# Optimization experiments

Hardware: AMD Instinct MI355X
Metric: run time of the kernel (lower is better)

## Reference

```python
import jax, jax.numpy as jnp
import numpy as np

NUM_CODES = 8192
CODE_DIM = 64
DECAY = 0.99
EPSILON = 1e-05
COMMITMENT_COST = 0.25


def setup_inputs() -> dict:
    key = jax.random.key(0)
    k1, k2, k3 = jax.random.split(key, 3)
    z = jax.random.normal(k1, (32768, CODE_DIM), dtype=jnp.float32)
    emb = jax.random.normal(k2, (NUM_CODES, CODE_DIM), dtype=jnp.float32)
    emb = emb / jnp.linalg.norm(emb, axis=1, keepdims=True)
    return {
        "z": z,
        "embedding": emb,
        "ema_cluster_size": jnp.zeros((NUM_CODES,), dtype=jnp.float32),
        "ema_embedding": emb.copy(),
    }


def reference(z, embedding, ema_cluster_size, ema_embedding):
    z_flat = z.reshape(-1, CODE_DIM)  # [N, D]
    # squared euclidean distances [N, K]
    distances = (
        jnp.sum(z_flat * z_flat, axis=1, keepdims=True)
        - 2.0 * (z_flat @ embedding.T)
        + jnp.sum(embedding * embedding, axis=1)
    )
    indices = jnp.argmin(distances, axis=1)  # [N] int
    z_q = embedding[indices]  # [N, D] gather

    # EMA buffer updates (training path), expressed as pure outputs.
    counts = jax.ops.segment_sum(
        jnp.ones_like(indices, dtype=z_flat.dtype), indices, num_segments=NUM_CODES
    )  # encodings.sum(0)
    dw = jax.ops.segment_sum(z_flat, indices, num_segments=NUM_CODES)  # encodings.T @ z_flat
    new_cluster_size = DECAY * ema_cluster_size + (1.0 - DECAY) * counts
    new_ema_embedding = DECAY * ema_embedding + (1.0 - DECAY) * dw
    n = jnp.sum(new_cluster_size)
    cluster_size = (new_cluster_size + EPSILON) / (n + NUM_CODES * EPSILON) * n
    new_embedding = new_ema_embedding / cluster_size[:, None]

    z_q_full = z_q.reshape(z.shape)
    z_q_st = z + jax.lax.stop_gradient(z_q_full - z)  # straight-through
    vq_loss = COMMITMENT_COST * jnp.mean(
        (jax.lax.stop_gradient(z_q_full) - z) ** 2
    )
    return (z_q_st, indices, vq_loss, new_embedding, new_cluster_size, new_ema_embedding)
```

## Files before the change

kernel.cpp:

```cpp
#include <hip/hip_runtime.h>

typedef _Float16 half8 __attribute__((ext_vector_type(8)));
typedef float f32x4 __attribute__((ext_vector_type(4)));

#define N_PTS   32768
#define DIMS    64
#define K_CODES 8192

#define OUT_ZQ      0
#define OUT_IDX     2097152
#define OUT_LOSS    2129920
#define OUT_NEWEMB  2129921
#define OUT_NCS     2654209
#define OUT_NEWEMA  2662401

#define SC_EHI      0
#define SC_ELO      262144
#define SC_ENSC     524288
#define SC_VAL1     532480
#define SC_IDX1     794624
#define SC_VAL2     1056768
#define SC_FIXLIST  1318912
#define SC_SORTED   1323008
#define SC_OFFSETS  1355776

#define WS_COUNTS   0
#define WS_CURSOR   8192
#define WS_LOSS     16384
#define WS_NSUM     16385
#define WS_FIXCNT   16386
#define WS_ZERO_BYTES (16388u * 4u)
#define WS_NCS      16388
#define WS_ENORM    24580
#define WS_IDX      32772
#define WS_DW       65540

#define MARGIN_SCALED 16.0f

__device__ inline void gld16(const void* g, void* l) {
    __builtin_amdgcn_global_load_lds((const __attribute__((address_space(1))) unsigned*)g,
                                     (__attribute__((address_space(3))) unsigned*)l, 16, 0, 0);
}
__device__ inline void gld4(const void* g, void* l) {
    __builtin_amdgcn_global_load_lds((const __attribute__((address_space(1))) unsigned*)g,
                                     (__attribute__((address_space(3))) unsigned*)l, 4, 0, 0);
}

__global__ __launch_bounds__(256) void esplit_kernel(const float* __restrict__ emb,
                                                     float4* __restrict__ ehi4,
                                                     float4* __restrict__ elo4,
                                                     float* __restrict__ ensc,
                                                     float* __restrict__ enorm) {
    int k = blockIdx.x * 256 + threadIdx.x;
    const float4* e4 = reinterpret_cast<const float4*>(emb + (size_t)k * DIMS);
    float vals[64];
    float sum = 0.0f;
#pragma unroll
    for (int i = 0; i < 16; ++i) {
        float4 v = e4[i];
        vals[i*4+0] = v.x; vals[i*4+1] = v.y; vals[i*4+2] = v.z; vals[i*4+3] = v.w;
        sum = fmaf(v.x, v.x, sum); sum = fmaf(v.y, v.y, sum);
        sum = fmaf(v.z, v.z, sum); sum = fmaf(v.w, v.w, sum);
    }
    enorm[k] = sum;
    ensc[k]  = 65536.0f * sum;
#pragma unroll
    for (int c = 0; c < 8; ++c) {
        union { _Float16 h[8]; float4 v; } uh, ul;
#pragma unroll
        for (int j = 0; j < 8; ++j) {
            float X = 256.0f * vals[c*8+j];
            _Float16 hh = (_Float16)X;
            uh.h[j] = hh;
            ul.h[j] = (_Float16)(X - (float)hh);
        }
        int cc = c ^ (k & 7);
        ehi4[(size_t)k*8 + cc] = uh.v;
        elo4[(size_t)k*8 + cc] = ul.v;
    }
}

__global__ __launch_bounds__(256) void argmin_mfma(const float* __restrict__ z,
                                                   const char* __restrict__ ehi_g,
                                                   const char* __restrict__ elo_g,
                                                   const float* __restrict__ ensc_g,
                                                   float* __restrict__ val1,
                                                   int* __restrict__ idx1,
                                                   float* __restrict__ val2) {
    __shared__ __align__(16) char ebuf[2][2][8192];
    __shared__ float enb[2][64];

    const int tid = threadIdx.x;
    const int w   = tid >> 6;
    const int l   = tid & 63;
    const int l15 = l & 15;
    const int l4  = l >> 4;
    const int bid = blockIdx.x;
    const int rowbase = (bid >> 2) * 128 + w * 32;
    const int c0      = (bid & 3) * 2048;

    half8 ahi[2][2], alo[2][2];
#pragma unroll
    for (int s = 0; s < 2; ++s) {
        const float* zp = z + (size_t)(rowbase + s*16 + l15) * DIMS + l4 * 8;
#pragma unroll
        for (int ks = 0; ks < 2; ++ks) {
            float4 z0 = *reinterpret_cast<const float4*>(zp + ks*32);
            float4 z1 = *reinterpret_cast<const float4*>(zp + ks*32 + 4);
            float xv[8] = {z0.x, z0.y, z0.z, z0.w, z1.x, z1.y, z1.z, z1.w};
            half8 h, lo;
#pragma unroll
            for (int j = 0; j < 8; ++j) {
                float X = -512.0f * xv[j];
                _Float16 hh = (_Float16)X;
                h[j]  = hh;
                lo[j] = (_Float16)(X - (float)hh);
            }
            ahi[s][ks] = h; alo[s][ks] = lo;
        }
    }

    float b1[8], b2[8]; int i1[8];
#pragma unroll
    for (int r = 0; r < 8; ++r) { b1[r] = 3.4e38f; b2[r] = 3.4e38f; i1[r] = 0; }

    int rdoff[2];
#pragma unroll
    for (int ks = 0; ks < 2; ++ks)
        rdoff[ks] = l15 * 128 + (((ks*4 + l4) ^ (l15 & 7)) * 16);

    {
        const size_t gb = (size_t)c0 * 128;
        const char* sh = ehi_g + gb + tid*16;
        const char* sl = elo_g + gb + tid*16;
        char* dh = &ebuf[0][0][0] + w*1024;
        char* dl = &ebuf[0][1][0] + w*1024;
        gld16(sh,        dh);        gld16(sh + 4096, dh + 4096);
        gld16(sl,        dl);        gld16(sl + 4096, dl + 4096);
        if (w == 0) gld4(ensc_g + c0 + l, &enb[0][0]);
    }
    __syncthreads();

    int b = 0;
    for (int ch = 0; ch < 32; ++ch) {
        if (ch < 31) {
            const size_t gb = (size_t)(c0 + (ch+1)*64) * 128;
            const char* sh = ehi_g + gb + tid*16;
            const char* sl = elo_g + gb + tid*16;
            char* dh = &ebuf[b^1][0][0] + w*1024;
            char* dl = &ebuf[b^1][1][0] + w*1024;
            gld16(sh,        dh);        gld16(sh + 4096, dh + 4096);
            gld16(sl,        dl);        gld16(sl + 4096, dl + 4096);
            if (w == 0) gld4(ensc_g + c0 + (ch+1)*64 + l, &enb[b^1][0]);
        }
        const char* bhbase = &ebuf[b][0][0];
        const char* blbase = &ebuf[b][1][0];
#pragma unroll
        for (int t = 0; t < 4; ++t) {
            float en = enb[b][t*16 + l15];
            f32x4 envec = (f32x4){en, en, en, en};
            half8 bh[2], bl[2];
#pragma unroll
            for (int ks = 0; ks < 2; ++ks) {
                bh[ks] = *reinterpret_cast<const half8*>(bhbase + t*2048 + rdoff[ks]);
                bl[ks] = *reinterpret_cast<const half8*>(blbase + t*2048 + rdoff[ks]);
            }
            f32x4 acc[2];
            __builtin_amdgcn_s_setprio(1);
#pragma unroll
            for (int s = 0; s < 2; ++s)
                acc[s] = __builtin_amdgcn_mfma_f32_16x16x32_f16(ahi[s][0], bh[0], envec, 0, 0, 0);
#pragma unroll
            for (int s = 0; s < 2; ++s)
                acc[s] = __builtin_amdgcn_mfma_f32_16x16x32_f16(ahi[s][0], bl[0], acc[s], 0, 0, 0);
#pragma unroll
            for (int s = 0; s < 2; ++s)
                acc[s] = __builtin_amdgcn_mfma_f32_16x16x32_f16(alo[s][0], bh[0], acc[s], 0, 0, 0);
#pragma unroll
            for (int s = 0; s < 2; ++s)
                acc[s] = __builtin_amdgcn_mfma_f32_16x16x32_f16(ahi[s][1], bh[1], acc[s], 0, 0, 0);
#pragma unroll
            for (int s = 0; s < 2; ++s)
                acc[s] = __builtin_amdgcn_mfma_f32_16x16x32_f16(ahi[s][1], bl[1], acc[s], 0, 0, 0);
#pragma unroll
            for (int s = 0; s < 2; ++s)
                acc[s] = __builtin_amdgcn_mfma_f32_16x16x32_f16(alo[s][1], bh[1], acc[s], 0, 0, 0);
            __builtin_amdgcn_s_setprio(0);

            const int code = c0 + ch*64 + t*16 + l15;
#pragma unroll
            for (int s = 0; s < 2; ++s) {
#pragma unroll
                for (int j = 0; j < 4; ++j) {
                    const int r = s*4 + j;
                    float v = acc[s][j];
                    float nb2;
                    asm("v_med3_f32 %0, %1, %2, %3"
                        : "=v"(nb2) : "v"(b1[r]), "v"(b2[r]), "v"(v));
                    b2[r] = nb2;
                    bool c = v < b1[r];
                    b1[r] = c ? v : b1[r];
                    i1[r] = c ? code : i1[r];
                }
            }
        }
        __syncthreads();
        b ^= 1;
    }

#pragma unroll
    for (int m = 1; m < 16; m <<= 1) {
#pragma unroll
        for (int r = 0; r < 8; ++r) {
            float ob1 = __shfl_xor(b1[r], m, 64);
            int   oi1 = __shfl_xor(i1[r], m, 64);
            float ob2 = __shfl_xor(b2[r], m, 64);
            float nb2 = fminf(fminf(b2[r], ob2), fmaxf(b1[r], ob1));
            bool take = (ob1 < b1[r]) || (ob1 == b1[r] && oi1 < i1[r]);
            b1[r] = take ? ob1 : b1[r];
            i1[r] = take ? oi1 : i1[r];
            b2[r] = nb2;
        }
    }
    if (l15 == 0) {
        const int cs = bid & 3;
#pragma unroll
        for (int s = 0; s < 2; ++s)
#pragma unroll
            for (int j = 0; j < 4; ++j) {
                int row = rowbase + s*16 + l4*4 + j;
                int o = cs * N_PTS + row;
                val1[o] = b1[s*4+j];
                idx1[o] = i1[s*4+j];
                val2[o] = b2[s*4+j];
            }
    }
}

__global__ __launch_bounds__(256) void combine_kernel(const float* __restrict__ val1,
                                                      const int* __restrict__ idx1,
                                                      const float* __restrict__ val2,
                                                      int* __restrict__ ws_idx,
                                                      float* __restrict__ out_idxf,
                                                      int* __restrict__ fixcnt,
                                                      int* __restrict__ fixlist,
                                                      float* __restrict__ counts) {
    int row = blockIdx.x * 256 + threadIdx.x;
    float b1 = val1[row]; int i1 = idx1[row]; float b2 = val2[row];
#pragma unroll
    for (int c = 1; c < 4; ++c) {
        float ob1 = val1[c*N_PTS + row];
        int   oi1 = idx1[c*N_PTS + row];
        float ob2 = val2[c*N_PTS + row];
        float nb2 = fminf(fminf(b2, ob2), fmaxf(b1, ob1));
        if (ob1 < b1) { b1 = ob1; i1 = oi1; }
        b2 = nb2;
    }
    ws_idx[row]   = i1;
    out_idxf[row] = (float)i1;
    atomicAdd(&counts[i1], 1.0f);
    if (b2 - b1 < MARGIN_SCALED) {
        int p = atomicAdd(fixcnt, 1);
        if (p < 4096) fixlist[p] = row;
    }
}

__global__ __launch_bounds__(256) void fixup_kernel(const float* __restrict__ z,
                                                    const float* __restrict__ emb,
                                                    const float* __restrict__ enorm,
                                                    const int* __restrict__ fixcnt,
                                                    const int* __restrict__ fixlist,
                                                    int* __restrict__ ws_idx,
                                                    float* __restrict__ out_idxf,
                                                    float* __restrict__ counts) {
    __shared__ float zrow[64];
    __shared__ float rv[256];
    __shared__ int   ri[256];
    int cnt = *fixcnt; if (cnt > 4096) cnt = 4096;
    for (int g = blockIdx.x; g < cnt; g += 64) {
        int row = fixlist[g];
        __syncthreads();
        if (threadIdx.x < 64) zrow[threadIdx.x] = z[(size_t)row * DIMS + threadIdx.x];
        __syncthreads();
        float best = 3.4e38f; int bi = 0;
        for (int k = threadIdx.x; k < K_CODES; k += 256) {
            const float4* e4 = reinterpret_cast<const float4*>(emb + (size_t)k * DIMS);
            float s = 0.0f;
#pragma unroll
            for (int i = 0; i < 16; ++i) {
                float4 ev = e4[i];
                s = fmaf(zrow[i*4+0], ev.x, s);
                s = fmaf(zrow[i*4+1], ev.y, s);
                s = fmaf(zrow[i*4+2], ev.z, s);
                s = fmaf(zrow[i*4+3], ev.w, s);
            }
            float d = fmaf(-2.0f, s, enorm[k]);
            if (d < best) { best = d; bi = k; }
        }
        rv[threadIdx.x] = best; ri[threadIdx.x] = bi;
        __syncthreads();
        for (int off = 128; off > 0; off >>= 1) {
            if (threadIdx.x < off) {
                float ov = rv[threadIdx.x + off]; int oi = ri[threadIdx.x + off];
                if (ov < rv[threadIdx.x] || (ov == rv[threadIdx.x] && oi < ri[threadIdx.x])) {
                    rv[threadIdx.x] = ov; ri[threadIdx.x] = oi;
                }
            }
            __syncthreads();
        }
        if (threadIdx.x == 0) {
            int old = ws_idx[row];
            if (ri[0] != old) {
                atomicAdd(&counts[old], -1.0f);
                atomicAdd(&counts[ri[0]], 1.0f);
                ws_idx[row] = ri[0];
                out_idxf[row] = (float)ri[0];
            }
        }
    }
}

__global__ __launch_bounds__(256) void scan_cs_kernel(const float* __restrict__ ema_cs,
                                                      const float* __restrict__ counts,
                                                      float* __restrict__ ncs_ws,
                                                      float* __restrict__ out_ncs,
                                                      float* __restrict__ nsum,
                                                      int* __restrict__ offsets) {
    __shared__ int excl[256];
    __shared__ int tot[256];
    __shared__ float fpart[256];
    const int t = threadIdx.x;
    const int base = t * 32;
    int loc[32];
    int run = 0;
    float fs = 0.0f;
#pragma unroll
    for (int i = 0; i < 32; ++i) {
        float c = counts[base + i];
        float v = fmaf(0.99f, ema_cs[base + i], 0.01f * c);
        ncs_ws[base + i] = v;
        out_ncs[base + i] = v;
        fs += v;
        loc[i] = run;
        run += (int)c;
    }
    tot[t] = run;
    fpart[t] = fs;
    __syncthreads();
    if (t == 0) {
        int r = 0;
        float f = 0.0f;
        for (int i = 0; i < 256; ++i) { excl[i] = r; r += tot[i]; f += fpart[i]; }
        nsum[0] = f;
    }
    __syncthreads();
    const int off = excl[t];
#pragma unroll
    for (int i = 0; i < 32; ++i) offsets[base + i] = off + loc[i];
}

__global__ __launch_bounds__(256) void place_kernel(const int* __restrict__ idx,
                                                    const int* __restrict__ offsets,
                                                    int* __restrict__ cursor,
                                                    int* __restrict__ sorted) {
    int p = blockIdx.x * 256 + threadIdx.x;
    int k = idx[p];
    int pos = offsets[k] + atomicAdd(&cursor[k], 1);
    sorted[pos] = p;
}

__global__ __launch_bounds__(256) void dw_kernel(const float* __restrict__ z,
                                                 const int* __restrict__ sorted,
                                                 const int* __restrict__ offsets,
                                                 const float* __restrict__ counts,
                                                 float* __restrict__ dw) {
    const int w = threadIdx.x >> 6;
    const int lane = threadIdx.x & 63;
    const int k = blockIdx.x * 4 + w;
    const int start = offsets[k];
    const int cnt = (int)counts[k];
    float s = 0.0f;
    for (int i = 0; i < cnt; ++i) {
        int p = sorted[start + i];
        s += z[(size_t)p * DIMS + lane];
    }
    dw[(size_t)k * DIMS + lane] = s;
}

__global__ __launch_bounds__(256) void scatter_light(const float* __restrict__ z,
                                                     const float* __restrict__ emb,
                                                     const int* __restrict__ idx,
                                                     float* __restrict__ zq_out,
                                                     float* __restrict__ loss_accum) {
    const int tid = threadIdx.x;
    const int p = blockIdx.x * 64 + (tid >> 2);
    const int q = tid & 3;
    const int k = idx[p];

    const float4* zp = reinterpret_cast<const float4*>(z + (size_t)p * DIMS + q * 16);
    const float4* ep = reinterpret_cast<const float4*>(emb + (size_t)k * DIMS + q * 16);
    float4* op = reinterpret_cast<float4*>(zq_out + (size_t)p * DIMS + q * 16);

    float lsum = 0.0f;
#pragma unroll
    for (int i = 0; i < 4; ++i) {
        float4 zv = zp[i];
        float4 ev = ep[i];
        float4 t;
        t.x = ev.x - zv.x; t.y = ev.y - zv.y; t.z = ev.z - zv.z; t.w = ev.w - zv.w;
        lsum = fmaf(t.x, t.x, lsum); lsum = fmaf(t.y, t.y, lsum);
        lsum = fmaf(t.z, t.z, lsum); lsum = fmaf(t.w, t.w, lsum);
        float4 o;
        o.x = zv.x + t.x; o.y = zv.y + t.y; o.z = zv.z + t.z; o.w = zv.w + t.w;
        op[i] = o;
    }
#pragma unroll
    for (int o = 32; o > 0; o >>= 1) lsum += __shfl_down(lsum, o);
    if ((tid & 63) == 0) atomicAdd(loss_accum, lsum);
}

__global__ __launch_bounds__(256) void final_kernel(const float* __restrict__ ema_emb,
                                                    const float* __restrict__ dw,
                                                    const float* __restrict__ ncs,
                                                    const float* __restrict__ n_ptr,
                                                    const float* __restrict__ loss_ptr,
                                                    float* __restrict__ out_newemb,
                                                    float* __restrict__ out_newema,
                                                    float* __restrict__ out_loss) {
    const int i = blockIdx.x * 256 + threadIdx.x;
    const int k = i >> 6;
    const float n = *n_ptr;
    const float cs = (ncs[k] + 1e-5f) / (n + (float)K_CODES * 1e-5f) * n;
    const float ne = fmaf(0.99f, ema_emb[i], 0.01f * dw[i]);
    out_newema[i] = ne;
    out_newemb[i] = ne / cs;
    if (i == 0) out_loss[0] = 0.25f * (loss_ptr[0] / 2097152.0f);
}

extern "C" void kernel_launch(void* const* d_in, const int* in_sizes, int n_in,
                              void* d_out, int out_size, void* d_ws, size_t ws_size,
                              hipStream_t stream) {
    const float* z       = (const float*)d_in[0];
    const float* emb     = (const float*)d_in[1];
    const float* ema_cs  = (const float*)d_in[2];
    const float* ema_emb = (const float*)d_in[3];
    float* out = (float*)d_out;
    float* ws  = (float*)d_ws;

    float* counts  = ws + WS_COUNTS;
    int*   cursor  = (int*)(ws + WS_CURSOR);
    float* loss    = ws + WS_LOSS;
    float* nsum    = ws + WS_NSUM;
    int*   fixcnt  = (int*)(ws + WS_FIXCNT);
    float* ncs     = ws + WS_NCS;
    float* enorm   = ws + WS_ENORM;
    int*   idx     = (int*)(ws + WS_IDX);
    float* dw      = ws + WS_DW;

    float* ehi     = out + SC_EHI;
    float* elo     = out + SC_ELO;
    float* ensc    = out + SC_ENSC;
    float* val1    = out + SC_VAL1;
    int*   idx1    = (int*)(out + SC_IDX1);
    float* val2    = out + SC_VAL2;
    int*   fixlist = (int*)(out + SC_FIXLIST);
    int*   sorted  = (int*)(out + SC_SORTED);
    int*   offsets = (int*)(out + SC_OFFSETS);

    hipMemsetAsync(d_ws, 0, WS_ZERO_BYTES, stream);

    esplit_kernel<<<K_CODES / 256, 256, 0, stream>>>(emb, (float4*)ehi, (float4*)elo, ensc, enorm);

    argmin_mfma<<<1024, 256, 0, stream>>>(z, (const char*)ehi, (const char*)elo, ensc,
                                          val1, idx1, val2);

    combine_kernel<<<N_PTS / 256, 256, 0, stream>>>(val1, idx1, val2, idx, out + OUT_IDX,
                                                    fixcnt, fixlist, counts);

    fixup_kernel<<<64, 256, 0, stream>>>(z, emb, enorm, fixcnt, fixlist, idx, out + OUT_IDX,
                                         counts);

    scan_cs_kernel<<<1, 256, 0, stream>>>(ema_cs, counts, ncs, out + OUT_NCS, nsum, offsets);

    place_kernel<<<N_PTS / 256, 256, 0, stream>>>(idx, offsets, cursor, sorted);

    dw_kernel<<<K_CODES / 4, 256, 0, stream>>>(z, sorted, offsets, counts, dw);

    scatter_light<<<N_PTS / 64, 256, 0, stream>>>(z, emb, idx, out + OUT_ZQ, loss);

    final_kernel<<<(K_CODES * DIMS) / 256, 256, 0, stream>>>(ema_emb, dw, ncs, nsum, loss,
                                                             out + OUT_NEWEMB,
                                                             out + OUT_NEWEMA,
                                                             out + OUT_LOSS);
}
```

Baseline: 304.6 us.

## Split argmin codebook eight ways and fuse dw accumulation into final EMA kernel

The MFMA argmin kernel now splits the codebook into eight slices of 1024 codes instead of four of 2048, and launches 2048 blocks. Each block streams 32-code chunks through half-sized LDS buffers, which lowers LDS use per block and gives the scheduler more resident blocks. The combine kernel merges eight partial best/second-best results instead of four, so it reads more scratch. Separately, the per-code dw segment-sum is fused into the final EMA/normalisation kernel, which drops one launch and the dw round trip through global memory. The sorted and offsets buffers move into workspace because the larger partial-result arrays now fill their old scratch space.

```diff
diff --git a/kernel.cpp b/kernel.cpp
--- a/kernel.cpp
+++ b/kernel.cpp
@@ -21,8 +21,6 @@
 #define SC_IDX1     794624
 #define SC_VAL2     1056768
 #define SC_FIXLIST  1318912
-#define SC_SORTED   1323008
-#define SC_OFFSETS  1355776
 
 #define WS_COUNTS   0
 #define WS_CURSOR   8192
@@ -33,7 +31,8 @@
 #define WS_NCS      16388
 #define WS_ENORM    24580
 #define WS_IDX      32772
-#define WS_DW       65540
+#define WS_SORTED   65540
+#define WS_OFFSETS  98308
 
 #define MARGIN_SCALED 16.0f
 
@@ -87,8 +86,8 @@
                                                    float* __restrict__ val1,
                                                    int* __restrict__ idx1,
                                                    float* __restrict__ val2) {
-    __shared__ __align__(16) char ebuf[2][2][8192];
-    __shared__ float enb[2][64];
+    __shared__ __align__(16) char ebuf[2][2][4096];
+    __shared__ float enb[2][32];
 
     const int tid = threadIdx.x;
     const int w   = tid >> 6;
@@ -96,8 +95,8 @@
     const int l15 = l & 15;
     const int l4  = l >> 4;
     const int bid = blockIdx.x;
-    const int rowbase = (bid >> 2) * 128 + w * 32;
-    const int c0      = (bid & 3) * 2048;
+    const int rowbase = (bid >> 3) * 128 + w * 32;
+    const int c0      = (bid & 7) * 1024;
 
     half8 ahi[2][2], alo[2][2];
 #pragma unroll
@@ -131,32 +130,24 @@
 
     {
         const size_t gb = (size_t)c0 * 128;
-        const char* sh = ehi_g + gb + tid*16;
-        const char* sl = elo_g + gb + tid*16;
-        char* dh = &ebuf[0][0][0] + w*1024;
-        char* dl = &ebuf[0][1][0] + w*1024;
-        gld16(sh,        dh);        gld16(sh + 4096, dh + 4096);
-        gld16(sl,        dl);        gld16(sl + 4096, dl + 4096);
-        if (w == 0) gld4(ensc_g + c0 + l, &enb[0][0]);
+        gld16(ehi_g + gb + tid*16, &ebuf[0][0][0] + w*1024);
+        gld16(elo_g + gb + tid*16, &ebuf[0][1][0] + w*1024);
+        if (w == 0 && l < 32) gld4(ensc_g + c0 + l, &enb[0][0]);
     }
     __syncthreads();
 
     int b = 0;
     for (int ch = 0; ch < 32; ++ch) {
         if (ch < 31) {
-            const size_t gb = (size_t)(c0 + (ch+1)*64) * 128;
-            const char* sh = ehi_g + gb + tid*16;
-            const char* sl = elo_g + gb + tid*16;
-            char* dh = &ebuf[b^1][0][0] + w*1024;
-            char* dl = &ebuf[b^1][1][0] + w*1024;
-            gld16(sh,        dh);        gld16(sh + 4096, dh + 4096);
-            gld16(sl,        dl);        gld16(sl + 4096, dl + 4096);
-            if (w == 0) gld4(ensc_g + c0 + (ch+1)*64 + l, &enb[b^1][0]);
+            const size_t gb = (size_t)(c0 + (ch+1)*32) * 128;
+            gld16(ehi_g + gb + tid*16, &ebuf[b^1][0][0] + w*1024);
+            gld16(elo_g + gb + tid*16, &ebuf[b^1][1][0] + w*1024);
+            if (w == 0 && l < 32) gld4(ensc_g + c0 + (ch+1)*32 + l, &enb[b^1][0]);
         }
         const char* bhbase = &ebuf[b][0][0];
         const char* blbase = &ebuf[b][1][0];
 #pragma unroll
-        for (int t = 0; t < 4; ++t) {
+        for (int t = 0; t < 2; ++t) {
             float en = enb[b][t*16 + l15];
             f32x4 envec = (f32x4){en, en, en, en};
             half8 bh[2], bl[2];
@@ -187,7 +178,7 @@
                 acc[s] = __builtin_amdgcn_mfma_f32_16x16x32_f16(alo[s][1], bh[1], acc[s], 0, 0, 0);
             __builtin_amdgcn_s_setprio(0);
 
-            const int code = c0 + ch*64 + t*16 + l15;
+            const int code = c0 + ch*32 + t*16 + l15;
 #pragma unroll
             for (int s = 0; s < 2; ++s) {
 #pragma unroll
@@ -223,7 +214,7 @@
         }
     }
     if (l15 == 0) {
-        const int cs = bid & 3;
+        const int cs = bid & 7;
 #pragma unroll
         for (int s = 0; s < 2; ++s)
 #pragma unroll
@@ -248,7 +239,7 @@
     int row = blockIdx.x * 256 + threadIdx.x;
     float b1 = val1[row]; int i1 = idx1[row]; float b2 = val2[row];
 #pragma unroll
-    for (int c = 1; c < 4; ++c) {
+    for (int c = 1; c < 8; ++c) {
         float ob1 = val1[c*N_PTS + row];
         int   oi1 = idx1[c*N_PTS + row];
         float ob2 = val2[c*N_PTS + row];
@@ -369,24 +360,6 @@
     sorted[pos] = p;
 }
 
-__global__ __launch_bounds__(256) void dw_kernel(const float* __restrict__ z,
-                                                 const int* __restrict__ sorted,
-                                                 const int* __restrict__ offsets,
-                                                 const float* __restrict__ counts,
-                                                 float* __restrict__ dw) {
-    const int w = threadIdx.x >> 6;
-    const int lane = threadIdx.x & 63;
-    const int k = blockIdx.x * 4 + w;
-    const int start = offsets[k];
-    const int cnt = (int)counts[k];
-    float s = 0.0f;
-    for (int i = 0; i < cnt; ++i) {
-        int p = sorted[start + i];
-        s += z[(size_t)p * DIMS + lane];
-    }
-    dw[(size_t)k * DIMS + lane] = s;
-}
-
 __global__ __launch_bounds__(256) void scatter_light(const float* __restrict__ z,
                                                      const float* __restrict__ emb,
                                                      const int* __restrict__ idx,
@@ -419,22 +392,34 @@
     if ((tid & 63) == 0) atomicAdd(loss_accum, lsum);
 }
 
-__global__ __launch_bounds__(256) void final_kernel(const float* __restrict__ ema_emb,
-                                                    const float* __restrict__ dw,
-                                                    const float* __restrict__ ncs,
-                                                    const float* __restrict__ n_ptr,
-                                                    const float* __restrict__ loss_ptr,
-                                                    float* __restrict__ out_newemb,
-                                                    float* __restrict__ out_newema,
-                                                    float* __restrict__ out_loss) {
-    const int i = blockIdx.x * 256 + threadIdx.x;
-    const int k = i >> 6;
+__global__ __launch_bounds__(256) void dw_final(const float* __restrict__ z,
+                                                const int* __restrict__ sorted,
+                                                const int* __restrict__ offsets,
+                                                const float* __restrict__ counts,
+                                                const float* __restrict__ ema_emb,
+                                                const float* __restrict__ ncs,
+                                                const float* __restrict__ n_ptr,
+                                                const float* __restrict__ loss_ptr,
+                                                float* __restrict__ out_newemb,
+                                                float* __restrict__ out_newema,
+                                                float* __restrict__ out_loss) {
+    const int w = threadIdx.x >> 6;
+    const int lane = threadIdx.x & 63;
+    const int k = blockIdx.x * 4 + w;
+    const int start = offsets[k];
+    const int cnt = (int)counts[k];
+    float s = 0.0f;
+    for (int i = 0; i < cnt; ++i) {
+        int p = sorted[start + i];
+        s += z[(size_t)p * DIMS + lane];
+    }
     const float n = *n_ptr;
     const float cs = (ncs[k] + 1e-5f) / (n + (float)K_CODES * 1e-5f) * n;
-    const float ne = fmaf(0.99f, ema_emb[i], 0.01f * dw[i]);
-    out_newema[i] = ne;
-    out_newemb[i] = ne / cs;
-    if (i == 0) out_loss[0] = 0.25f * (loss_ptr[0] / 2097152.0f);
+    const float ne = fmaf(0.99f, ema_emb[(size_t)k * DIMS + lane], 0.01f * s);
+    out_newema[(size_t)k * DIMS + lane] = ne;
+    out_newemb[(size_t)k * DIMS + lane] = ne / cs;
+    if (blockIdx.x == 0 && threadIdx.x == 0)
+        out_loss[0] = 0.25f * (loss_ptr[0] / 2097152.0f);
 }
 
 extern "C" void kernel_launch(void* const* d_in, const int* in_sizes, int n_in,
@@ -455,7 +440,8 @@
     float* ncs     = ws + WS_NCS;
     float* enorm   = ws + WS_ENORM;
     int*   idx     = (int*)(ws + WS_IDX);
-    float* dw      = ws + WS_DW;
+    int*   sorted  = (int*)(ws + WS_SORTED);
+    int*   offsets = (int*)(ws + WS_OFFSETS);
 
     float* ehi     = out + SC_EHI;
     float* elo     = out + SC_ELO;
@@ -464,14 +450,12 @@
     int*   idx1    = (int*)(out + SC_IDX1);
     float* val2    = out + SC_VAL2;
     int*   fixlist = (int*)(out + SC_FIXLIST);
-    int*   sorted  = (int*)(out + SC_SORTED);
-    int*   offsets = (int*)(out + SC_OFFSETS);
 
     hipMemsetAsync(d_ws, 0, WS_ZERO_BYTES, stream);
 
     esplit_kernel<<<K_CODES / 256, 256, 0, stream>>>(emb, (float4*)ehi, (float4*)elo, ensc, enorm);
 
-    argmin_mfma<<<1024, 256, 0, stream>>>(z, (const char*)ehi, (const char*)elo, ensc,
+    argmin_mfma<<<2048, 256, 0, stream>>>(z, (const char*)ehi, (const char*)elo, ensc,
                                           val1, idx1, val2);
 
     combine_kernel<<<N_PTS / 256, 256, 0, stream>>>(val1, idx1, val2, idx, out + OUT_IDX,
@@ -484,12 +468,10 @@
 
     place_kernel<<<N_PTS / 256, 256, 0, stream>>>(idx, offsets, cursor, sorted);
 
-    dw_kernel<<<K_CODES / 4, 256, 0, stream>>>(z, sorted, offsets, counts, dw);
-
     scatter_light<<<N_PTS / 64, 256, 0, stream>>>(z, emb, idx, out + OUT_ZQ, loss);
 
-    final_kernel<<<(K_CODES * DIMS) / 256, 256, 0, stream>>>(ema_emb, dw, ncs, nsum, loss,
-                                                             out + OUT_NEWEMB,
-                                                             out + OUT_NEWEMA,
-                                                             out + OUT_LOSS);
-}
+    dw_final<<<K_CODES / 4, 256, 0, stream>>>(z, sorted, offsets, counts, ema_emb, ncs,
+                                              nsum, loss,
+                                              out + OUT_NEWEMB, out + OUT_NEWEMA,
+                                              out + OUT_LOSS);
+}
```

Result: no change. 308.8 us (+1.4%).
